# Kernel tuning notes

Measured on AMD Instinct MI355X. Metric: run time of the kernel, lower is better.

## Reference

```python
import jax, jax.numpy as jnp
import numpy as np

RC = 5.0          # radial cutoff
NB = 8            # number of Gaussian radial basis functions
NPATH = 11        # graph-conv tensor-product paths (in_way, r_way, n_contract)->out_way
NORM_FACTOR = 10.0


def setup_inputs() -> dict:
    key = jax.random.key(0)
    ks = jax.random.split(key, 24)
    N, E, C = 20000, 200000, 32
    s = 1.0 / np.sqrt(C)
    inp = {
        "rij": jax.random.normal(ks[0], (E, 3), jnp.float32) * 1.5,
        "node_x0": jax.random.normal(ks[1], (N, C), jnp.float32),
        "node_x1": jax.random.normal(ks[2], (N, C, 3), jnp.float32),
        "node_x2": jax.random.normal(ks[3], (N, C, 3, 3), jnp.float32),
        "idx_i": jax.random.randint(ks[4], (E,), 0, N, jnp.int32),
        "idx_j": jax.random.randint(ks[5], (E,), 0, N, jnp.int32),
        # radial filter MLP (rbf -> per-path per-channel filters)
        "W_rbf": jax.random.normal(ks[6], (NB, NPATH * C), jnp.float32) / np.sqrt(NB),
        "b_rbf": jax.random.normal(ks[7], (NPATH * C,), jnp.float32) * 0.1,
        # multi-body self-interaction: channel mixing per way + pair-path couplings
        "Wmix0": jax.random.normal(ks[8], (C, C), jnp.float32) * s,
        "Wmix1": jax.random.normal(ks[9], (C, C), jnp.float32) * s,
        "Wmix2": jax.random.normal(ks[10], (C, C), jnp.float32) * s,
        "coupling": jax.random.normal(ks[11], (8, C), jnp.float32) * 0.1,
        # gated nonlinearity params (gates computed from way-0 features)
        "Wg0": jax.random.normal(ks[12], (C, C), jnp.float32) * s,
        "Wg1": jax.random.normal(ks[13], (C, C), jnp.float32) * s,
        "Wg2": jax.random.normal(ks[14], (C, C), jnp.float32) * s,
        "bg0": jnp.zeros((C,), jnp.float32),
        "bg1": jnp.zeros((C,), jnp.float32),
        "bg2": jnp.zeros((C,), jnp.float32),
    }
    return inp


def _forward(rij, node_x0, node_x1, node_x2, idx_i, idx_j,
             W_rbf, b_rbf, Wmix0, Wmix1, Wmix2, coupling,
             Wg0, Wg1, Wg2, bg0, bg1, bg2):
    N, C = node_x0.shape
    # --- radial filters ---
    d = jnp.maximum(jnp.linalg.norm(rij, axis=-1), 1e-6)            # [E]
    rhat = rij / d[:, None]                                         # [E,3]
    centers = jnp.linspace(0.0, RC, NB)
    rbf = jnp.exp(-((d[:, None] - centers) ** 2) / 0.25)            # [E,NB]
    fc = 0.5 * (jnp.cos(jnp.pi * jnp.minimum(d, RC) / RC) + 1.0)    # cosine cutoff
    filt = ((rbf @ W_rbf + b_rbf) * fc[:, None]).reshape(-1, NPATH, C)  # [E,P,C]

    # --- graph conv (conv_mode='node_j'): gather neighbor tensors, tensor-product with rhat ---
    xj0 = node_x0[idx_j]                                            # [E,C]
    xj1 = node_x1[idx_j]                                            # [E,C,3]
    xj2 = node_x2[idx_j]                                            # [E,C,3,3]
    x1r = jnp.einsum('eca,ea->ec', xj1, rhat)                       # v.rhat

    m0 = filt[:, 0] * xj0
    m0 += filt[:, 5] * x1r
    m0 += filt[:, 10] * jnp.einsum('ecab,ea,eb->ec', xj2, rhat, rhat)

    m1 = jnp.einsum('ec,ea->eca', filt[:, 1] * xj0, rhat)
    m1 += filt[:, 3][:, :, None] * xj1
    m1 += jnp.einsum('ec,ea->eca', filt[:, 6] * x1r, rhat)
    m1 += filt[:, 8][:, :, None] * jnp.einsum('ecab,eb->eca', xj2, rhat)

    m2 = jnp.einsum('ec,ea,eb->ecab', filt[:, 2] * xj0, rhat, rhat)
    m2 += jnp.einsum('eca,eb->ecab', filt[:, 4][:, :, None] * xj1, rhat)
    m2 += filt[:, 7][:, :, None, None] * xj2
    m2 += filt[:, 9][:, :, None, None] * jnp.einsum('ecab,eb,ed->ecad', xj2, rhat, rhat)

    # --- scatter-add aggregation per way + normalization ---
    a0 = jax.ops.segment_sum(m0, idx_i, num_segments=N) / NORM_FACTOR
    a1 = jax.ops.segment_sum(m1, idx_i, num_segments=N) / NORM_FACTOR
    a2 = jax.ops.segment_sum(m2, idx_i, num_segments=N) / NORM_FACTOR

    # --- multi-body self-interaction (channel mix + pairwise tensor contractions) ---
    cp = coupling
    y0 = a0 @ Wmix0 \
        + cp[0] * (a0 * a0) \
        + cp[3] * jnp.einsum('nca,nca->nc', a1, a1) \
        + cp[6] * jnp.einsum('ncab,ncab->nc', a2, a2)
    y1 = jnp.einsum('nca,cd->nda', a1, Wmix1) \
        + cp[1][None, :, None] * a0[:, :, None] * a1 \
        + cp[5][None, :, None] * jnp.einsum('ncab,ncb->nca', a2, a1)
    y2 = jnp.einsum('ncab,cd->ndab', a2, Wmix2) \
        + cp[2][None, :, None, None] * a0[:, :, None, None] * a2 \
        + cp[4][None, :, None, None] * jnp.einsum('nca,ncb->ncab', a1, a1) \
        + cp[7][None, :, None, None] * jnp.einsum('ncab,ncbd->ncad', a2, a2)

    # --- gated nonlinearity (scalar channel drives gates for higher ways) ---
    z0 = jax.nn.silu(y0 @ Wg0 + bg0)
    z1 = y1 * jax.nn.silu(y0 @ Wg1 + bg1)[:, :, None]
    z2 = y2 * jax.nn.silu(y0 @ Wg2 + bg2)[:, :, None, None]

    # --- residual add (res_add) ---
    o0 = node_x0 + z0
    o1 = node_x1 + z1
    o2 = node_x2 + z2
    # pack dict {0,1,2} outputs into one array [N,C,1+3+9]
    return jnp.concatenate([o0[:, :, None], o1, o2.reshape(N, C, 9)], axis=-1)


def reference(rij, node_x0, node_x1, node_x2, idx_i, idx_j,
              W_rbf, b_rbf, Wmix0, Wmix1, Wmix2, coupling,
              Wg0, Wg1, Wg2, bg0, bg1, bg2):
    return _forward(rij, node_x0, node_x1, node_x2, idx_i, idx_j,
                    W_rbf, b_rbf, Wmix0, Wmix1, Wmix2, coupling,
                    Wg0, Wg1, Wg2, bg0, bg1, bg2)
```

## Files before the change

kernel.cpp:

```cpp
#include <hip/hip_runtime.h>
#include <cmath>

#define CH 32
#define NBASIS 8
#define NPATH 11
#define NF 13
#define NPF (NF * CH)
#define MAXDEG 40
#define NW 4

typedef unsigned int u32;
typedef __fp16 half2_t __attribute__((ext_vector_type(2)));

#define SM_SREC_OFF 5632
#define SM_SY0_OFF  6656
#define SMEM_TOTAL  10752

__device__ __forceinline__ float silu_f(float x) {
    return x / (1.0f + __expf(-x));
}

__device__ __forceinline__ u32 bf16r(float x) {
    return (__float_as_uint(x) + 0x8000u) >> 16;
}
__device__ __forceinline__ float bf16lo(u32 w) {
    return __uint_as_float(w << 16);
}
__device__ __forceinline__ float bf16hi(u32 w) {
    return __uint_as_float(w & 0xffff0000u);
}

__device__ __forceinline__ u32 f16pk(float a, float b) {
    union { half2_t h; u32 u; } cv;
    cv.h = __builtin_amdgcn_cvt_pkrtz(a, b);
    return cv.u;
}
__device__ __forceinline__ half2_t ash2(u32 w) {
    union { u32 u; half2_t h; } cv; cv.u = w; return cv.h;
}

#if __has_builtin(__builtin_amdgcn_fdot2)
__device__ __forceinline__ float dot2f(u32 a, u32 b, float c) {
    return __builtin_amdgcn_fdot2(ash2(a), ash2(b), c, false);
}
#else
__device__ __forceinline__ float dot2f(u32 a, u32 b, float c) {
    half2_t ha = ash2(a), hb = ash2(b);
    c = fmaf((float)ha.x, (float)hb.x, c);
    c = fmaf((float)ha.y, (float)hb.y, c);
    return c;
}
#endif

__device__ __forceinline__ void gload_lds16(const void* g, void* l) {
    __builtin_amdgcn_global_load_lds(
        (const __attribute__((address_space(1))) void*)g,
        (__attribute__((address_space(3))) void*)l, 16, 0, 0);
}

__global__ __launch_bounds__(256) void prep_kernel(
    const float* __restrict__ x0,
    const float* __restrict__ x1,
    const float* __restrict__ x2,
    uint4* __restrict__ xph4,
    const float* __restrict__ rij,
    const int*   __restrict__ idx_i,
    const int*   __restrict__ idx_j,
    int*    __restrict__ cnt,
    float4* __restrict__ recs,
    int N, int E, int ablocks)
{
    if ((int)blockIdx.x < ablocks) {
        int t = blockIdx.x * 256 + threadIdx.x;
        if (t >= N * CH) return;

        float f[13];
        f[0] = x0[t];
        const float* p1 = x1 + (size_t)t * 3;
#pragma unroll
        for (int a = 0; a < 3; a++) f[1 + a] = p1[a];
        const float* p2 = x2 + (size_t)t * 9;
#pragma unroll
        for (int q = 0; q < 9; q++) f[4 + q] = p2[q];

        u32 d[8];
#pragma unroll
        for (int qp = 0; qp < 6; qp++)
            d[qp] = bf16r(f[2 * qp]) | (bf16r(f[2 * qp + 1]) << 16);
        d[6] = bf16r(f[12]);
        d[7] = 0u;
        uint4* xo = xph4 + (size_t)t * 2;
        xo[0] = make_uint4(d[0], d[1], d[2], d[3]);
        xo[1] = make_uint4(d[4], d[5], d[6], d[7]);
    } else {
        int e = ((int)blockIdx.x - ablocks) * 256 + threadIdx.x;
        if (e >= E) return;

        float rx = rij[e * 3 + 0], ry = rij[e * 3 + 1], rz = rij[e * 3 + 2];
        float dn = sqrtf(rx * rx + ry * ry + rz * rz);
        float d = fmaxf(dn, 1e-6f);
        float inv = 1.0f / d;

        float rbf[NBASIS];
#pragma unroll
        for (int k = 0; k < NBASIS; k++) {
            float ck = 5.0f * (float)k / (float)(NBASIS - 1);
            float del = d - ck;
            rbf[k] = __expf(-4.0f * del * del);
        }
        float dc = fminf(d, 5.0f);
        float fc = 0.5f * (__cosf((float)M_PI * dc * 0.2f) + 1.0f);
        float scale = fc * 0.1f;

        int i = idx_i[e];
        int pos = atomicAdd(&cnt[i], 1);
        if (pos >= MAXDEG) return;

        u32 w3  = ((u32)idx_j[e] << 16) | bf16r(scale);
        u32 p01 = f16pk(rbf[0] * scale, rbf[1] * scale);
        u32 p23 = f16pk(rbf[2] * scale, rbf[3] * scale);
        u32 p45 = f16pk(rbf[4] * scale, rbf[5] * scale);
        u32 p67 = f16pk(rbf[6] * scale, rbf[7] * scale);

        float4* r = recs + 2 * (size_t)(i * MAXDEG + pos);
        r[0] = make_float4(rx * inv, ry * inv, rz * inv, __uint_as_float(w3));
        r[1] = make_float4(__uint_as_float(p01), __uint_as_float(p23),
                           __uint_as_float(p45), __uint_as_float(p67));
    }
}

__global__ __launch_bounds__(256, 1) void edge_node_kernel(
    const float4*   __restrict__ recs,
    const uint4*    __restrict__ xph4,
    const int*      __restrict__ cnt,
    const float*    __restrict__ W_rbf,
    const float*    __restrict__ b_rbf,
    const float* __restrict__ x0,
    const float* __restrict__ x1,
    const float* __restrict__ x2,
    const float* __restrict__ Wmix0, const float* __restrict__ Wmix1,
    const float* __restrict__ Wmix2,
    const float* __restrict__ coupling,
    const float* __restrict__ Wg0, const float* __restrict__ Wg1,
    const float* __restrict__ Wg2,
    const float* __restrict__ bg0, const float* __restrict__ bg1,
    const float* __restrict__ bg2,
    float* __restrict__ out, int N)
{
    __shared__ __align__(16) char smem[SMEM_TOTAL];
    uint4*  sW4  = (uint4*)smem;
    float4* srec = (float4*)(smem + SM_SREC_OFF);
    float*  sA   = (float*)smem;
    float*  sy0  = (float*)(smem + SM_SY0_OFF);

    int tid  = threadIdx.x;
    int wid  = tid >> 6;
    int lane = tid & 63;
    int half = lane >> 5;
    int c    = lane & 31;
    int n    = blockIdx.x * NW + wid;
    bool valid = (n < N);
    int nn = valid ? n : (N - 1);

    const char* gbase = (const char*)(recs + 2 * (size_t)nn * MAXDEG);
    {
        char* lbase = (char*)(srec + (size_t)wid * (MAXDEG * 2));
        gload_lds16(gbase + lane * 16, lbase);
        if (lane < 16)
            gload_lds16(gbase + 1024 + lane * 16, lbase + 1024);
    }

    const u32* recw = (const u32*)gbase;
    u32 w30 = recw[half * 8 + 3];
    u32 w31 = recw[(half + 2) * 8 + 3];
    u32 w32 = recw[(half + 4) * 8 + 3];
    int deg_g = cnt[nn];

#pragma unroll
    for (int i = 0; i < 2; i++) {
        int idx = tid + i * 256;
        if (idx < NPATH * CH) {
            int cc = idx & 31, p = idx >> 5;
            const float* w = W_rbf + p * CH + cc;
            uint4 v;
            v.x = f16pk(w[0 * NPATH * CH], w[1 * NPATH * CH]);
            v.y = f16pk(w[2 * NPATH * CH], w[3 * NPATH * CH]);
            v.z = f16pk(w[4 * NPATH * CH], w[5 * NPATH * CH]);
            v.w = f16pk(w[6 * NPATH * CH], w[7 * NPATH * CH]);
            sW4[idx] = v;
        }
    }

    float breg[NPATH];
#pragma unroll
    for (int p = 0; p < NPATH; p++) breg[p] = b_rbf[p * CH + c];

    auto gath = [&](uint4& ga, uint4& gb, u32 w3) {
        int j = (int)(w3 >> 16);
        j = j < N ? j : N - 1;
        const uint4* g = xph4 + (((size_t)j * CH + c) << 1);
        ga = g[0];
        gb = g[1];
    };

    uint4 G0a, G0b, G1a, G1b, G2a, G2b;
    gath(G0a, G0b, w30);
    gath(G1a, G1b, w31);
    gath(G2a, G2b, w32);

    __syncthreads();

    int deg = valid ? (deg_g < MAXDEG ? deg_g : MAXDEG) : 0;

    int s0 = half, s1 = half + 2, s2 = half + 4;
    bool v0 = s0 < deg, v1 = s1 < deg, v2 = s2 < deg;

    float A0 = 0.0f, A1[3] = {0, 0, 0}, A2[9] = {0, 0, 0, 0, 0, 0, 0, 0, 0};

    const uint4* sW4c = sW4 + c;

    auto compute = [&](float4 ra, float4 rb4, uint4 ga, uint4 gb) {
        float G[13];
        G[0]  = bf16lo(ga.x); G[1]  = bf16hi(ga.x);
        G[2]  = bf16lo(ga.y); G[3]  = bf16hi(ga.y);
        G[4]  = bf16lo(ga.z); G[5]  = bf16hi(ga.z);
        G[6]  = bf16lo(ga.w); G[7]  = bf16hi(ga.w);
        G[8]  = bf16lo(gb.x); G[9]  = bf16hi(gb.x);
        G[10] = bf16lo(gb.y); G[11] = bf16hi(gb.y);
        G[12] = bf16lo(gb.z);

        float scale = bf16lo(__float_as_uint(ra.w));
        u32 pb0 = __float_as_uint(rb4.x), pb1 = __float_as_uint(rb4.y),
            pb2 = __float_as_uint(rb4.z), pb3 = __float_as_uint(rb4.w);

        float fv[NPATH];
#pragma unroll
        for (int p = 0; p < NPATH; p++) {
            uint4 wp = sW4c[p * CH];
            float acc = scale * breg[p];
            acc = dot2f(pb0, wp.x, acc);
            acc = dot2f(pb1, wp.y, acc);
            acc = dot2f(pb2, wp.z, acc);
            acc = dot2f(pb3, wp.w, acc);
            fv[p] = acc;
        }

        float hv[3] = {ra.x, ra.y, ra.z};
        float xj0 = G[0];
        float xv[3] = {G[1], G[2], G[3]};
        float x1r = xv[0] * hv[0] + xv[1] * hv[1] + xv[2] * hv[2];
        float x2r[3];
#pragma unroll
        for (int a = 0; a < 3; a++)
            x2r[a] = G[4 + a * 3 + 0] * hv[0] + G[4 + a * 3 + 1] * hv[1]
                   + G[4 + a * 3 + 2] * hv[2];
        float x2rr = x2r[0] * hv[0] + x2r[1] * hv[1] + x2r[2] * hv[2];

        A0 += fv[0] * xj0 + fv[5] * x1r + fv[10] * x2rr;

        float s01 = fv[1] * xj0 + fv[6] * x1r;
#pragma unroll
        for (int a = 0; a < 3; a++)
            A1[a] += s01 * hv[a] + fv[3] * xv[a] + fv[8] * x2r[a];

        float f2x = fv[2] * xj0;
#pragma unroll
        for (int a = 0; a < 3; a++) {
            float w = f2x * hv[a] + fv[4] * xv[a] + fv[9] * x2r[a];
#pragma unroll
            for (int b = 0; b < 3; b++)
                A2[a * 3 + b] += w * hv[b] + fv[7] * G[4 + a * 3 + b];
        }
    };

    const float4* sr = srec + (size_t)wid * (MAXDEG * 2);

    while (v0) {
        bool n0 = (s0 + 6 < deg);
        bool n1 = v1 && (s1 + 6 < deg);
        bool n2 = v2 && (s2 + 6 < deg);

        float4 ra0 = sr[2 * s0], rb0 = sr[2 * s0 + 1];
        int t0 = s0 + 6 < MAXDEG ? s0 + 6 : MAXDEG - 1;
        u32 w0n = __float_as_uint(sr[2 * t0].w);
        float4 ra1, rb1, ra2, rb2;
        u32 w1n = 0, w2n = 0;
        if (v1) {
            ra1 = sr[2 * s1]; rb1 = sr[2 * s1 + 1];
            int t1 = s1 + 6 < MAXDEG ? s1 + 6 : MAXDEG - 1;
            w1n = __float_as_uint(sr[2 * t1].w);
        }
        if (v2) {
            ra2 = sr[2 * s2]; rb2 = sr[2 * s2 + 1];
            int t2 = s2 + 6 < MAXDEG ? s2 + 6 : MAXDEG - 1;
            w2n = __float_as_uint(sr[2 * t2].w);
        }

        compute(ra0, rb0, G0a, G0b);
        if (n0) gath(G0a, G0b, w0n);
        s0 += 6; v0 = n0;

        if (v1) {
            compute(ra1, rb1, G1a, G1b);
            if (n1) gath(G1a, G1b, w1n);
            s1 += 6; v1 = n1;
        }
        if (v2) {
            compute(ra2, rb2, G2a, G2b);
            if (n2) gath(G2a, G2b, w2n);
            s2 += 6; v2 = n2;
        }
    }

    A0 += __shfl_xor(A0, 32);
#pragma unroll
    for (int a = 0; a < 3; a++) A1[a] += __shfl_xor(A1[a], 32);
#pragma unroll
    for (int q = 0; q < 9; q++) A2[q] += __shfl_xor(A2[q], 32);

    __syncthreads();

    {
        float* an = sA + wid * NPF;
        if (half == 0) {
            an[c] = A0;
#pragma unroll
            for (int a = 0; a < 3; a++) an[(1 + a) * CH + c] = A1[a];
        } else {
#pragma unroll
            for (int q = 0; q < 9; q++) an[(4 + q) * CH + c] = A2[q];
        }
    }
    __syncthreads();

    int nl = (tid >> 5) & 3;
    int d  = tid & 31;
    int ng = blockIdx.x * NW + nl;
    bool phA = (tid < 128);
    bool act = (ng < N);
    const float* An = sA + nl * NPF;

    float a0d = An[d];
    float a1d[3], a2d[9];
#pragma unroll
    for (int a = 0; a < 3; a++) a1d[a] = An[(1 + a) * CH + d];
#pragma unroll
    for (int q = 0; q < 9; q++) a2d[q] = An[(4 + q) * CH + d];

    float y2[9] = {0, 0, 0, 0, 0, 0, 0, 0, 0};
    if (phA) {
        float y0 = 0.0f;
#pragma unroll 8
        for (int cc = 0; cc < CH; cc++)
            y0 = fmaf(An[cc], Wmix0[cc * CH + d], y0);
        float cp0 = coupling[0 * CH + d], cp3 = coupling[3 * CH + d],
              cp6 = coupling[6 * CH + d];
        float n1v = a1d[0] * a1d[0] + a1d[1] * a1d[1] + a1d[2] * a1d[2];
        float n2v = 0.0f;
#pragma unroll
        for (int q = 0; q < 9; q++) n2v = fmaf(a2d[q], a2d[q], n2v);
        y0 += cp0 * a0d * a0d + cp3 * n1v + cp6 * n2v;
        sy0[nl * CH + d] = y0;
    } else {
#pragma unroll 4
        for (int cc = 0; cc < CH; cc++) {
            float w2 = Wmix2[cc * CH + d];
#pragma unroll
            for (int q = 0; q < 9; q++)
                y2[q] = fmaf(An[(4 + q) * CH + cc], w2, y2[q]);
        }
    }
    __syncthreads();

    if (act && phA) {
        float y1[3] = {0, 0, 0};
#pragma unroll 4
        for (int cc = 0; cc < CH; cc++) {
            float w1 = Wmix1[cc * CH + d];
#pragma unroll
            for (int a = 0; a < 3; a++)
                y1[a] = fmaf(An[(1 + a) * CH + cc], w1, y1[a]);
        }
        float cp1 = coupling[1 * CH + d], cp5 = coupling[5 * CH + d];
#pragma unroll
        for (int a = 0; a < 3; a++) {
            float a2a1 = a2d[a * 3 + 0] * a1d[0] + a2d[a * 3 + 1] * a1d[1]
                       + a2d[a * 3 + 2] * a1d[2];
            y1[a] += cp1 * a0d * a1d[a] + cp5 * a2a1;
        }

        float g0 = bg0[d], g1 = bg1[d];
#pragma unroll 8
        for (int cc = 0; cc < CH; cc++) {
            float yv = sy0[nl * CH + cc];
            g0 = fmaf(yv, Wg0[cc * CH + d], g0);
            g1 = fmaf(yv, Wg1[cc * CH + d], g1);
        }
        g0 = silu_f(g0);
        g1 = silu_f(g1);

        const float* xs0 = x0 + (size_t)ng * CH;
        const float* xs1 = x1 + ((size_t)ng * CH + d) * 3;
        float* o = out + (size_t)ng * NPF + d * NF;
        o[0] = xs0[d] + g0;
#pragma unroll
        for (int a = 0; a < 3; a++)
            o[1 + a] = xs1[a] + y1[a] * g1;
    } else if (act) {
        float cp2 = coupling[2 * CH + d], cp4 = coupling[4 * CH + d],
              cp7 = coupling[7 * CH + d];
#pragma unroll
        for (int a = 0; a < 3; a++) {
#pragma unroll
            for (int b = 0; b < 3; b++) {
                float a2a2 = a2d[a * 3 + 0] * a2d[0 * 3 + b]
                           + a2d[a * 3 + 1] * a2d[1 * 3 + b]
                           + a2d[a * 3 + 2] * a2d[2 * 3 + b];
                y2[a * 3 + b] += cp2 * a0d * a2d[a * 3 + b]
                               + cp4 * a1d[a] * a1d[b] + cp7 * a2a2;
            }
        }

        float g2 = bg2[d];
#pragma unroll 8
        for (int cc = 0; cc < CH; cc++)
            g2 = fmaf(sy0[nl * CH + cc], Wg2[cc * CH + d], g2);
        g2 = silu_f(g2);

        const float* xs2 = x2 + ((size_t)ng * CH + d) * 9;
        float* o = out + (size_t)ng * NPF + d * NF;
#pragma unroll
        for (int q = 0; q < 9; q++)
            o[4 + q] = xs2[q] + y2[q] * g2;
    }
}

extern "C" void kernel_launch(void* const* d_in, const int* in_sizes, int n_in,
                              void* d_out, int out_size, void* d_ws, size_t ws_size,
                              hipStream_t stream) {
    const float* rij      = (const float*)d_in[0];
    const float* x0       = (const float*)d_in[1];
    const float* x1       = (const float*)d_in[2];
    const float* x2       = (const float*)d_in[3];
    const int*   idx_i    = (const int*)d_in[4];
    const int*   idx_j    = (const int*)d_in[5];
    const float* W_rbf    = (const float*)d_in[6];
    const float* b_rbf    = (const float*)d_in[7];
    const float* Wmix0    = (const float*)d_in[8];
    const float* Wmix1    = (const float*)d_in[9];
    const float* Wmix2    = (const float*)d_in[10];
    const float* coupling = (const float*)d_in[11];
    const float* Wg0      = (const float*)d_in[12];
    const float* Wg1      = (const float*)d_in[13];
    const float* Wg2      = (const float*)d_in[14];
    const float* bg0      = (const float*)d_in[15];
    const float* bg1      = (const float*)d_in[16];
    const float* bg2      = (const float*)d_in[17];

    int E = in_sizes[4];
    int N = in_sizes[1] / CH;

    float4* recs = (float4*)d_ws;
    uint4*  xph4 = (uint4*)(recs + 2 * (size_t)N * MAXDEG);
    int*    cnt  = (int*)(xph4 + (size_t)N * CH * 2);

    hipMemsetAsync(cnt, 0, (size_t)N * sizeof(int), stream);

    int ablocks = (N * CH + 255) / 256;
    int fblocks = (E + 255) / 256;
    prep_kernel<<<ablocks + fblocks, 256, 0, stream>>>(
        x0, x1, x2, xph4, rij, idx_i, idx_j, cnt, recs, N, E, ablocks);

    edge_node_kernel<<<(N + NW - 1) / NW, 256, 0, stream>>>(
        recs, xph4, cnt, W_rbf, b_rbf, x0, x1, x2,
        Wmix0, Wmix1, Wmix2, coupling, Wg0, Wg1, Wg2, bg0, bg1, bg2,
        (float*)d_out, N);
}
```

Before: 220.9 us.

## Replace LDS staging and block barriers with wave-local readlane broadcasts in epilogue

```diff
diff --git a/kernel.cpp b/kernel.cpp
--- a/kernel.cpp
+++ b/kernel.cpp
@@ -13,7 +13,6 @@
 typedef __fp16 half2_t __attribute__((ext_vector_type(2)));
 
 #define SM_SREC_OFF 5632
-#define SM_SY0_OFF  6656
 #define SMEM_TOTAL  10752
 
 __device__ __forceinline__ float silu_f(float x) {
@@ -51,6 +50,10 @@
     return c;
 }
 #endif
+
+__device__ __forceinline__ float rl32(float v, int l) {
+    return __uint_as_float(__builtin_amdgcn_readlane(__float_as_uint(v), l));
+}
 
 __device__ __forceinline__ void gload_lds16(const void* g, void* l) {
     __builtin_amdgcn_global_load_lds(
@@ -150,8 +153,6 @@
     __shared__ __align__(16) char smem[SMEM_TOTAL];
     uint4*  sW4  = (uint4*)smem;
     float4* srec = (float4*)(smem + SM_SREC_OFF);
-    float*  sA   = (float*)smem;
-    float*  sy0  = (float*)(smem + SM_SY0_OFF);
 
     int tid  = threadIdx.x;
     int wid  = tid >> 6;
@@ -318,117 +319,89 @@
 #pragma unroll
     for (int q = 0; q < 9; q++) A2[q] += __shfl_xor(A2[q], 32);
 
-    __syncthreads();
-
+    if (!valid) return;
+
+    int d = c;
+
+    float y0 = 0.0f;
+#pragma unroll 8
+    for (int cc = 0; cc < CH; cc++)
+        y0 = fmaf(rl32(A0, cc), Wmix0[cc * CH + d], y0);
     {
-        float* an = sA + wid * NPF;
-        if (half == 0) {
-            an[c] = A0;
-#pragma unroll
-            for (int a = 0; a < 3; a++) an[(1 + a) * CH + c] = A1[a];
-        } else {
-#pragma unroll
-            for (int q = 0; q < 9; q++) an[(4 + q) * CH + c] = A2[q];
-        }
-    }
-    __syncthreads();
-
-    int nl = (tid >> 5) & 3;
-    int d  = tid & 31;
-    int ng = blockIdx.x * NW + nl;
-    bool phA = (tid < 128);
-    bool act = (ng < N);
-    const float* An = sA + nl * NPF;
-
-    float a0d = An[d];
-    float a1d[3], a2d[9];
-#pragma unroll
-    for (int a = 0; a < 3; a++) a1d[a] = An[(1 + a) * CH + d];
-#pragma unroll
-    for (int q = 0; q < 9; q++) a2d[q] = An[(4 + q) * CH + d];
-
-    float y2[9] = {0, 0, 0, 0, 0, 0, 0, 0, 0};
-    if (phA) {
-        float y0 = 0.0f;
-#pragma unroll 8
-        for (int cc = 0; cc < CH; cc++)
-            y0 = fmaf(An[cc], Wmix0[cc * CH + d], y0);
         float cp0 = coupling[0 * CH + d], cp3 = coupling[3 * CH + d],
               cp6 = coupling[6 * CH + d];
-        float n1v = a1d[0] * a1d[0] + a1d[1] * a1d[1] + a1d[2] * a1d[2];
+        float n1v = A1[0] * A1[0] + A1[1] * A1[1] + A1[2] * A1[2];
         float n2v = 0.0f;
 #pragma unroll
-        for (int q = 0; q < 9; q++) n2v = fmaf(a2d[q], a2d[q], n2v);
-        y0 += cp0 * a0d * a0d + cp3 * n1v + cp6 * n2v;
-        sy0[nl * CH + d] = y0;
-    } else {
-#pragma unroll 4
-        for (int cc = 0; cc < CH; cc++) {
-            float w2 = Wmix2[cc * CH + d];
-#pragma unroll
-            for (int q = 0; q < 9; q++)
-                y2[q] = fmaf(An[(4 + q) * CH + cc], w2, y2[q]);
-        }
-    }
-    __syncthreads();
-
-    if (act && phA) {
+        for (int q = 0; q < 9; q++) n2v = fmaf(A2[q], A2[q], n2v);
+        y0 += cp0 * A0 * A0 + cp3 * n1v + cp6 * n2v;
+    }
+
+    float* o = out + (size_t)n * NPF + d * NF;
+
+    if (half == 0) {
         float y1[3] = {0, 0, 0};
 #pragma unroll 4
         for (int cc = 0; cc < CH; cc++) {
             float w1 = Wmix1[cc * CH + d];
-#pragma unroll
-            for (int a = 0; a < 3; a++)
-                y1[a] = fmaf(An[(1 + a) * CH + cc], w1, y1[a]);
+            y1[0] = fmaf(rl32(A1[0], cc), w1, y1[0]);
+            y1[1] = fmaf(rl32(A1[1], cc), w1, y1[1]);
+            y1[2] = fmaf(rl32(A1[2], cc), w1, y1[2]);
         }
         float cp1 = coupling[1 * CH + d], cp5 = coupling[5 * CH + d];
 #pragma unroll
         for (int a = 0; a < 3; a++) {
-            float a2a1 = a2d[a * 3 + 0] * a1d[0] + a2d[a * 3 + 1] * a1d[1]
-                       + a2d[a * 3 + 2] * a1d[2];
-            y1[a] += cp1 * a0d * a1d[a] + cp5 * a2a1;
+            float a2a1 = A2[a * 3 + 0] * A1[0] + A2[a * 3 + 1] * A1[1]
+                       + A2[a * 3 + 2] * A1[2];
+            y1[a] += cp1 * A0 * A1[a] + cp5 * a2a1;
         }
 
         float g0 = bg0[d], g1 = bg1[d];
 #pragma unroll 8
         for (int cc = 0; cc < CH; cc++) {
-            float yv = sy0[nl * CH + cc];
+            float yv = rl32(y0, cc);
             g0 = fmaf(yv, Wg0[cc * CH + d], g0);
             g1 = fmaf(yv, Wg1[cc * CH + d], g1);
         }
         g0 = silu_f(g0);
         g1 = silu_f(g1);
 
-        const float* xs0 = x0 + (size_t)ng * CH;
-        const float* xs1 = x1 + ((size_t)ng * CH + d) * 3;
-        float* o = out + (size_t)ng * NPF + d * NF;
+        const float* xs0 = x0 + (size_t)n * CH;
+        const float* xs1 = x1 + ((size_t)n * CH + d) * 3;
         o[0] = xs0[d] + g0;
 #pragma unroll
         for (int a = 0; a < 3; a++)
             o[1 + a] = xs1[a] + y1[a] * g1;
-    } else if (act) {
+    } else {
+        float y2[9] = {0, 0, 0, 0, 0, 0, 0, 0, 0};
+#pragma unroll 4
+        for (int cc = 0; cc < CH; cc++) {
+            float w2 = Wmix2[cc * CH + d];
+#pragma unroll
+            for (int q = 0; q < 9; q++)
+                y2[q] = fmaf(rl32(A2[q], cc), w2, y2[q]);
+        }
         float cp2 = coupling[2 * CH + d], cp4 = coupling[4 * CH + d],
               cp7 = coupling[7 * CH + d];
 #pragma unroll
         for (int a = 0; a < 3; a++) {
 #pragma unroll
             for (int b = 0; b < 3; b++) {
-                float a2a2 = a2d[a * 3 + 0] * a2d[0 * 3 + b]
-                           + a2d[a * 3 + 1] * a2d[1 * 3 + b]
-                           + a2d[a * 3 + 2] * a2d[2 * 3 + b];
-                y2[a * 3 + b] += cp2 * a0d * a2d[a * 3 + b]
-                               + cp4 * a1d[a] * a1d[b] + cp7 * a2a2;
+                float a2a2 = A2[a * 3 + 0] * A2[0 * 3 + b]
+                           + A2[a * 3 + 1] * A2[1 * 3 + b]
+                           + A2[a * 3 + 2] * A2[2 * 3 + b];
+                y2[a * 3 + b] += cp2 * A0 * A2[a * 3 + b]
+                               + cp4 * A1[a] * A1[b] + cp7 * a2a2;
             }
         }
 
         float g2 = bg2[d];
 #pragma unroll 8
         for (int cc = 0; cc < CH; cc++)
-            g2 = fmaf(sy0[nl * CH + cc], Wg2[cc * CH + d], g2);
+            g2 = fmaf(rl32(y0, cc), Wg2[cc * CH + d], g2);
         g2 = silu_f(g2);
 
-        const float* xs2 = x2 + ((size_t)ng * CH + d) * 9;
-        float* o = out + (size_t)ng * NPF + d * NF;
+        const float* xs2 = x2 + ((size_t)n * CH + d) * 9;
 #pragma unroll
         for (int q = 0; q < 9; q++)
             o[4 + q] = xs2[q] + y2[q] * g2;
```

Result: slower. 276.8 us (+25.3%).
